# Kernel optimization log

Hardware: AMD Instinct MI355X
Metric: run time of the kernel (lower is better)

## Reference

```python
import jax, jax.numpy as jnp
import numpy as np

B = 4096
FEAT = 40960
HID = 1024
L1 = 64
L2 = 32
P_ACTIVE = 30.0 / FEAT  # ~30 active features per position


def setup_inputs() -> dict:
    key = jax.random.key(0)
    ks = jax.random.split(key, 12)
    # Sparse binary HalfKP-style features
    white_features = (jax.random.uniform(ks[0], (B, FEAT)) < P_ACTIVE).astype(jnp.float32)
    black_features = (jax.random.uniform(ks[1], (B, FEAT)) < P_ACTIVE).astype(jnp.float32)
    stm = (jax.random.uniform(ks[2], (B, 1)) < 0.5).astype(jnp.float32)
    s = 0.02
    params = {
        'ft_w': jax.random.normal(ks[3], (HID, FEAT), jnp.float32) * s,
        'ft_b': jax.random.normal(ks[4], (HID,), jnp.float32) * s,
        'l1_w': jax.random.normal(ks[5], (L1, 2 * HID), jnp.float32) * s,
        'l1_b': jax.random.normal(ks[6], (L1,), jnp.float32) * s,
        'l2_w': jax.random.normal(ks[7], (L2, L1), jnp.float32) * s,
        'l2_b': jax.random.normal(ks[8], (L2,), jnp.float32) * s,
        'l3_w': jax.random.normal(ks[9], (1, L2), jnp.float32) * s,
        'l3_b': jax.random.normal(ks[10], (1,), jnp.float32) * s,
    }
    return dict(white_features=white_features, black_features=black_features, stm=stm, **params)


def reference(white_features, black_features, stm,
              ft_w, ft_b, l1_w, l1_b, l2_w, l2_b, l3_w, l3_b):
    # Feature transformer (shared weights, both perspectives)
    w = white_features @ ft_w.T + ft_b  # [B, HID]
    b = black_features @ ft_w.T + ft_b  # [B, HID]
    wb = jnp.concatenate([w, b], axis=1)  # [B, 2*HID]
    bw = jnp.concatenate([b, w], axis=1)
    acc = stm * wb + (1.0 - stm) * bw
    h1 = jnp.clip(acc, 0.0, 1.0)
    h2 = jnp.clip(h1 @ l1_w.T + l1_b, 0.0, 1.0)
    h3 = jnp.clip(h2 @ l2_w.T + l2_b, 0.0, 1.0)
    raw = h3 @ l3_w.T + l3_b  # [B, 1]
    return jax.nn.sigmoid(raw), raw
```

## Files before the change

kernel.cpp:

```cpp
#include <hip/hip_runtime.h>
#include <hip/hip_bf16.h>

#define B_SZ 4096
#define FEAT 40960
#define HID  1024
#define L1N  64
#define L2N  32
#define IDX_CAP 512

static __device__ __forceinline__ unsigned short f2bf(float x) {
    __hip_bfloat16 h = __float2bfloat16(x);
    return *reinterpret_cast<unsigned short*>(&h);
}
static __device__ __forceinline__ float bf2f(unsigned short u) {
    unsigned int v = ((unsigned int)u) << 16;
    return __uint_as_float(v);
}
static __device__ __forceinline__ float clipf(float x) {
    return fminf(fmaxf(x, 0.0f), 1.0f);
}

__global__ __launch_bounds__(256) void transpose_ftw(
    const float* __restrict__ ftw, unsigned short* __restrict__ ftwT) {
    __shared__ float tile[32][33];
    int tx = threadIdx.x, ty = threadIdx.y;
    int f0 = blockIdx.x * 32;
    int h0 = blockIdx.y * 32;
#pragma unroll
    for (int i = 0; i < 4; ++i) {
        int h = h0 + ty + 8 * i;
        tile[ty + 8 * i][tx] = ftw[(size_t)h * FEAT + f0 + tx];
    }
    __syncthreads();
#pragma unroll
    for (int i = 0; i < 4; ++i) {
        int f = f0 + ty + 8 * i;
        ftwT[(size_t)f * HID + h0 + tx] = f2bf(tile[tx][ty + 8 * i]);
    }
}

__global__ __launch_bounds__(256) void ft_kernel(
    const float* __restrict__ wf, const float* __restrict__ bfeat,
    const float* __restrict__ stm, const unsigned short* __restrict__ ftwT,
    const float* __restrict__ ftb, unsigned short* __restrict__ h1) {

    __shared__ int w_idx[IDX_CAP];
    __shared__ int b_idx[IDX_CAP];
    __shared__ int cnt_w, cnt_b;

    const int t = threadIdx.x;
    const int b = blockIdx.x;

    if (t == 0) { cnt_w = 0; cnt_b = 0; }
    __syncthreads();

    const float4* wf4 = (const float4*)(wf + (size_t)b * FEAT);
    const float4* bf4 = (const float4*)(bfeat + (size_t)b * FEAT);
    for (int it = 0; it < (FEAT / 4) / 256; ++it) {
        int i4 = it * 256 + t;
        float4 wv = wf4[i4];
        float4 bv = bf4[i4];
        int base = i4 * 4;
        if (wv.x != 0.f) { int p = atomicAdd(&cnt_w, 1); if (p < IDX_CAP) w_idx[p] = base + 0; }
        if (wv.y != 0.f) { int p = atomicAdd(&cnt_w, 1); if (p < IDX_CAP) w_idx[p] = base + 1; }
        if (wv.z != 0.f) { int p = atomicAdd(&cnt_w, 1); if (p < IDX_CAP) w_idx[p] = base + 2; }
        if (wv.w != 0.f) { int p = atomicAdd(&cnt_w, 1); if (p < IDX_CAP) w_idx[p] = base + 3; }
        if (bv.x != 0.f) { int p = atomicAdd(&cnt_b, 1); if (p < IDX_CAP) b_idx[p] = base + 0; }
        if (bv.y != 0.f) { int p = atomicAdd(&cnt_b, 1); if (p < IDX_CAP) b_idx[p] = base + 1; }
        if (bv.z != 0.f) { int p = atomicAdd(&cnt_b, 1); if (p < IDX_CAP) b_idx[p] = base + 2; }
        if (bv.w != 0.f) { int p = atomicAdd(&cnt_b, 1); if (p < IDX_CAP) b_idx[p] = base + 3; }
    }
    __syncthreads();
    const int nw = min(cnt_w, IDX_CAP);
    const int nb = min(cnt_b, IDX_CAP);

    float4 bias = ((const float4*)ftb)[t];
    float aw0 = bias.x, aw1 = bias.y, aw2 = bias.z, aw3 = bias.w;
    float ab0 = bias.x, ab1 = bias.y, ab2 = bias.z, ab3 = bias.w;

    for (int i = 0; i < nw; ++i) {
        int f = w_idx[i];
        ushort4 u = ((const ushort4*)(ftwT + (size_t)f * HID))[t];
        aw0 += bf2f(u.x); aw1 += bf2f(u.y); aw2 += bf2f(u.z); aw3 += bf2f(u.w);
    }
    for (int i = 0; i < nb; ++i) {
        int f = b_idx[i];
        ushort4 u = ((const ushort4*)(ftwT + (size_t)f * HID))[t];
        ab0 += bf2f(u.x); ab1 += bf2f(u.y); ab2 += bf2f(u.z); ab3 += bf2f(u.w);
    }

    const bool wfirst = (stm[b] != 0.0f);
    float f0 = wfirst ? aw0 : ab0, f1 = wfirst ? aw1 : ab1;
    float f2 = wfirst ? aw2 : ab2, f3 = wfirst ? aw3 : ab3;
    float s0 = wfirst ? ab0 : aw0, s1 = wfirst ? ab1 : aw1;
    float s2 = wfirst ? ab2 : aw2, s3 = wfirst ? ab3 : aw3;

    ushort4 of, os;
    of.x = f2bf(clipf(f0)); of.y = f2bf(clipf(f1)); of.z = f2bf(clipf(f2)); of.w = f2bf(clipf(f3));
    os.x = f2bf(clipf(s0)); os.y = f2bf(clipf(s1)); os.z = f2bf(clipf(s2)); os.w = f2bf(clipf(s3));

    ((ushort4*)(h1 + (size_t)b * 2 * HID))[t]       = of;
    ((ushort4*)(h1 + (size_t)b * 2 * HID + HID))[t] = os;
}

__global__ __launch_bounds__(256) void mlp_kernel(
    const unsigned short* __restrict__ h1,
    const float* __restrict__ l1w, const float* __restrict__ l1b,
    const float* __restrict__ l2w, const float* __restrict__ l2b,
    const float* __restrict__ l3w, const float* __restrict__ l3b,
    float* __restrict__ out) {

    const int ROWS = 4;
    __shared__ float  h1s[4][2 * HID];
    __shared__ float4 part[4 * L1N];
    __shared__ float  h2s[4][L1N];
    __shared__ float  h3s[4][L2N];

    const int t = threadIdx.x;
    const int r0 = blockIdx.x * ROWS;

    for (int r = 0; r < ROWS; ++r) {
        const ushort4* src = (const ushort4*)(h1 + (size_t)(r0 + r) * 2 * HID);
        ushort4 u0 = src[t];
        ushort4 u1 = src[256 + t];
        h1s[r][4 * t + 0] = bf2f(u0.x); h1s[r][4 * t + 1] = bf2f(u0.y);
        h1s[r][4 * t + 2] = bf2f(u0.z); h1s[r][4 * t + 3] = bf2f(u0.w);
        h1s[r][1024 + 4 * t + 0] = bf2f(u1.x); h1s[r][1024 + 4 * t + 1] = bf2f(u1.y);
        h1s[r][1024 + 4 * t + 2] = bf2f(u1.z); h1s[r][1024 + 4 * t + 3] = bf2f(u1.w);
    }
    __syncthreads();

    {
        const int k = t & 63, p = t >> 6;
        float a0 = 0.f, a1 = 0.f, a2 = 0.f, a3 = 0.f;
        const float4* w4 = (const float4*)(l1w + (size_t)k * 2 * HID + (size_t)p * 512);
        const int jbase = p * 512;
        for (int jj = 0; jj < 128; ++jj) {
            float4 w = w4[jj];
            int j = jbase + jj * 4;
            a0 += w.x * h1s[0][j] + w.y * h1s[0][j + 1] + w.z * h1s[0][j + 2] + w.w * h1s[0][j + 3];
            a1 += w.x * h1s[1][j] + w.y * h1s[1][j + 1] + w.z * h1s[1][j + 2] + w.w * h1s[1][j + 3];
            a2 += w.x * h1s[2][j] + w.y * h1s[2][j + 1] + w.z * h1s[2][j + 2] + w.w * h1s[2][j + 3];
            a3 += w.x * h1s[3][j] + w.y * h1s[3][j + 1] + w.z * h1s[3][j + 2] + w.w * h1s[3][j + 3];
        }
        part[p * L1N + k] = make_float4(a0, a1, a2, a3);
    }
    __syncthreads();
    if (t < L1N) {
        float4 s0 = part[t], s1 = part[L1N + t], s2 = part[2 * L1N + t], s3 = part[3 * L1N + t];
        float bias = l1b[t];
        h2s[0][t] = clipf(s0.x + s1.x + s2.x + s3.x + bias);
        h2s[1][t] = clipf(s0.y + s1.y + s2.y + s3.y + bias);
        h2s[2][t] = clipf(s0.z + s1.z + s2.z + s3.z + bias);
        h2s[3][t] = clipf(s0.w + s1.w + s2.w + s3.w + bias);
    }
    __syncthreads();

    if (t < ROWS * L2N) {
        int r = t >> 5, k2 = t & 31;
        float a = l2b[k2];
        for (int j = 0; j < L1N; ++j) a += h2s[r][j] * l2w[k2 * L1N + j];
        h3s[r][k2] = clipf(a);
    }
    __syncthreads();

    if (t < ROWS) {
        float raw = l3b[0];
        for (int j = 0; j < L2N; ++j) raw += h3s[t][j] * l3w[j];
        float sig = 1.0f / (1.0f + expf(-raw));
        out[r0 + t] = sig;
        out[B_SZ + r0 + t] = raw;
    }
}

extern "C" void kernel_launch(void* const* d_in, const int* in_sizes, int n_in,
                              void* d_out, int out_size, void* d_ws, size_t ws_size,
                              hipStream_t stream) {
    const float* wf    = (const float*)d_in[0];
    const float* bfeat = (const float*)d_in[1];
    const float* stm   = (const float*)d_in[2];
    const float* ftw   = (const float*)d_in[3];
    const float* ftb   = (const float*)d_in[4];
    const float* l1w   = (const float*)d_in[5];
    const float* l1b   = (const float*)d_in[6];
    const float* l2w   = (const float*)d_in[7];
    const float* l2b   = (const float*)d_in[8];
    const float* l3w   = (const float*)d_in[9];
    const float* l3b   = (const float*)d_in[10];
    float* out = (float*)d_out;

    unsigned short* ftwT = (unsigned short*)d_ws;
    unsigned short* h1   = ftwT + (size_t)FEAT * HID;

    transpose_ftw<<<dim3(FEAT / 32, HID / 32), dim3(32, 8), 0, stream>>>(ftw, ftwT);
    ft_kernel<<<B_SZ, 256, 0, stream>>>(wf, bfeat, stm, ftwT, ftb, h1);
    mlp_kernel<<<B_SZ / 4, 256, 0, stream>>>(h1, l1w, l1b, l2w, l2b, l3w, l3b, out);
}
```

Baseline: 1.459 ms.

## Fuse feature transformer with MLP and widen transpose tiles with packed bf16 stores

The sparse feature-transformer kernel and the MLP kernel are merged into one kernel that handles four rows per block, so the bf16 h1 intermediate is kept in shared memory in fp32 instead of being written to and re-read from global memory. The transpose kernel now uses 32x64 tiles and writes packed pairs of bf16 values as 32-bit stores. The fused kernel has a quarter as many blocks as the old feature-transformer kernel, and each block scans four rows serially. This lowers parallelism and raises shared-memory use, which could hurt latency hiding on the memory-bound feature scan. IDX_CAP is also reduced to 128 indices per row.

After: 1.515 ms. 1.04x slower.

```diff
diff --git a/kernel.cpp b/kernel.cpp
--- a/kernel.cpp
+++ b/kernel.cpp
@@ -6,7 +6,8 @@
 #define HID  1024
 #define L1N  64
 #define L2N  32
-#define IDX_CAP 512
+#define IDX_CAP 128
+#define ROWS 4
 
 static __device__ __forceinline__ unsigned short f2bf(float x) {
     __hip_bfloat16 h = __float2bfloat16(x);
@@ -22,111 +23,101 @@
 
 __global__ __launch_bounds__(256) void transpose_ftw(
     const float* __restrict__ ftw, unsigned short* __restrict__ ftwT) {
-    __shared__ float tile[32][33];
-    int tx = threadIdx.x, ty = threadIdx.y;
-    int f0 = blockIdx.x * 32;
-    int h0 = blockIdx.y * 32;
+    __shared__ float tile[32][65];
+    const int tx = threadIdx.x;
+    const int ty = threadIdx.y;
+    const int f0 = blockIdx.x * 32;
+    const int h0 = blockIdx.y * 64;
 #pragma unroll
-    for (int i = 0; i < 4; ++i) {
-        int h = h0 + ty + 8 * i;
-        tile[ty + 8 * i][tx] = ftw[(size_t)h * FEAT + f0 + tx];
+    for (int i = 0; i < 8; ++i) {
+        int h = ty + 8 * i;
+        tile[tx][h] = ftw[(size_t)(h0 + h) * FEAT + f0 + tx];
     }
     __syncthreads();
 #pragma unroll
     for (int i = 0; i < 4; ++i) {
-        int f = f0 + ty + 8 * i;
-        ftwT[(size_t)f * HID + h0 + tx] = f2bf(tile[tx][ty + 8 * i]);
+        int f = ty + 8 * i;
+        float a = tile[f][2 * tx];
+        float b = tile[f][2 * tx + 1];
+        unsigned int pk = (unsigned int)f2bf(a) | ((unsigned int)f2bf(b) << 16);
+        ((unsigned int*)(ftwT + (size_t)(f0 + f) * HID + h0))[tx] = pk;
     }
 }
 
-__global__ __launch_bounds__(256) void ft_kernel(
+__global__ __launch_bounds__(256) void nnue_fused(
     const float* __restrict__ wf, const float* __restrict__ bfeat,
     const float* __restrict__ stm, const unsigned short* __restrict__ ftwT,
-    const float* __restrict__ ftb, unsigned short* __restrict__ h1) {
-
-    __shared__ int w_idx[IDX_CAP];
-    __shared__ int b_idx[IDX_CAP];
-    __shared__ int cnt_w, cnt_b;
-
-    const int t = threadIdx.x;
-    const int b = blockIdx.x;
-
-    if (t == 0) { cnt_w = 0; cnt_b = 0; }
-    __syncthreads();
-
-    const float4* wf4 = (const float4*)(wf + (size_t)b * FEAT);
-    const float4* bf4 = (const float4*)(bfeat + (size_t)b * FEAT);
-    for (int it = 0; it < (FEAT / 4) / 256; ++it) {
-        int i4 = it * 256 + t;
-        float4 wv = wf4[i4];
-        float4 bv = bf4[i4];
-        int base = i4 * 4;
-        if (wv.x != 0.f) { int p = atomicAdd(&cnt_w, 1); if (p < IDX_CAP) w_idx[p] = base + 0; }
-        if (wv.y != 0.f) { int p = atomicAdd(&cnt_w, 1); if (p < IDX_CAP) w_idx[p] = base + 1; }
-        if (wv.z != 0.f) { int p = atomicAdd(&cnt_w, 1); if (p < IDX_CAP) w_idx[p] = base + 2; }
-        if (wv.w != 0.f) { int p = atomicAdd(&cnt_w, 1); if (p < IDX_CAP) w_idx[p] = base + 3; }
-        if (bv.x != 0.f) { int p = atomicAdd(&cnt_b, 1); if (p < IDX_CAP) b_idx[p] = base + 0; }
-        if (bv.y != 0.f) { int p = atomicAdd(&cnt_b, 1); if (p < IDX_CAP) b_idx[p] = base + 1; }
-        if (bv.z != 0.f) { int p = atomicAdd(&cnt_b, 1); if (p < IDX_CAP) b_idx[p] = base + 2; }
-        if (bv.w != 0.f) { int p = atomicAdd(&cnt_b, 1); if (p < IDX_CAP) b_idx[p] = base + 3; }
-    }
-    __syncthreads();
-    const int nw = min(cnt_w, IDX_CAP);
-    const int nb = min(cnt_b, IDX_CAP);
-
-    float4 bias = ((const float4*)ftb)[t];
-    float aw0 = bias.x, aw1 = bias.y, aw2 = bias.z, aw3 = bias.w;
-    float ab0 = bias.x, ab1 = bias.y, ab2 = bias.z, ab3 = bias.w;
-
-    for (int i = 0; i < nw; ++i) {
-        int f = w_idx[i];
-        ushort4 u = ((const ushort4*)(ftwT + (size_t)f * HID))[t];
-        aw0 += bf2f(u.x); aw1 += bf2f(u.y); aw2 += bf2f(u.z); aw3 += bf2f(u.w);
-    }
-    for (int i = 0; i < nb; ++i) {
-        int f = b_idx[i];
-        ushort4 u = ((const ushort4*)(ftwT + (size_t)f * HID))[t];
-        ab0 += bf2f(u.x); ab1 += bf2f(u.y); ab2 += bf2f(u.z); ab3 += bf2f(u.w);
-    }
-
-    const bool wfirst = (stm[b] != 0.0f);
-    float f0 = wfirst ? aw0 : ab0, f1 = wfirst ? aw1 : ab1;
-    float f2 = wfirst ? aw2 : ab2, f3 = wfirst ? aw3 : ab3;
-    float s0 = wfirst ? ab0 : aw0, s1 = wfirst ? ab1 : aw1;
-    float s2 = wfirst ? ab2 : aw2, s3 = wfirst ? ab3 : aw3;
-
-    ushort4 of, os;
-    of.x = f2bf(clipf(f0)); of.y = f2bf(clipf(f1)); of.z = f2bf(clipf(f2)); of.w = f2bf(clipf(f3));
-    os.x = f2bf(clipf(s0)); os.y = f2bf(clipf(s1)); os.z = f2bf(clipf(s2)); os.w = f2bf(clipf(s3));
-
-    ((ushort4*)(h1 + (size_t)b * 2 * HID))[t]       = of;
-    ((ushort4*)(h1 + (size_t)b * 2 * HID + HID))[t] = os;
-}
-
-__global__ __launch_bounds__(256) void mlp_kernel(
-    const unsigned short* __restrict__ h1,
+    const float* __restrict__ ftb,
     const float* __restrict__ l1w, const float* __restrict__ l1b,
     const float* __restrict__ l2w, const float* __restrict__ l2b,
     const float* __restrict__ l3w, const float* __restrict__ l3b,
     float* __restrict__ out) {
 
-    const int ROWS = 4;
-    __shared__ float  h1s[4][2 * HID];
+    __shared__ int  idx[2][ROWS][IDX_CAP];
+    __shared__ int  cnt[2][ROWS];
+    __shared__ float h1s[ROWS][2 * HID];
     __shared__ float4 part[4 * L1N];
-    __shared__ float  h2s[4][L1N];
-    __shared__ float  h3s[4][L2N];
+    __shared__ float h2s[ROWS][L1N];
+    __shared__ float h3s[ROWS][L2N];
 
     const int t = threadIdx.x;
     const int r0 = blockIdx.x * ROWS;
 
+    if (t < 2 * ROWS) ((int*)cnt)[t] = 0;
+    __syncthreads();
+
     for (int r = 0; r < ROWS; ++r) {
-        const ushort4* src = (const ushort4*)(h1 + (size_t)(r0 + r) * 2 * HID);
-        ushort4 u0 = src[t];
-        ushort4 u1 = src[256 + t];
-        h1s[r][4 * t + 0] = bf2f(u0.x); h1s[r][4 * t + 1] = bf2f(u0.y);
-        h1s[r][4 * t + 2] = bf2f(u0.z); h1s[r][4 * t + 3] = bf2f(u0.w);
-        h1s[r][1024 + 4 * t + 0] = bf2f(u1.x); h1s[r][1024 + 4 * t + 1] = bf2f(u1.y);
-        h1s[r][1024 + 4 * t + 2] = bf2f(u1.z); h1s[r][1024 + 4 * t + 3] = bf2f(u1.w);
+        const float4* wf4 = (const float4*)(wf + (size_t)(r0 + r) * FEAT);
+        const float4* bf4 = (const float4*)(bfeat + (size_t)(r0 + r) * FEAT);
+        for (int it = 0; it < (FEAT / 4) / 256; ++it) {
+            int i4 = it * 256 + t;
+            float4 wv = wf4[i4];
+            float4 bv = bf4[i4];
+            int base = i4 * 4;
+            if (wv.x != 0.f) { int p = atomicAdd(&cnt[0][r], 1); if (p < IDX_CAP) idx[0][r][p] = base + 0; }
+            if (wv.y != 0.f) { int p = atomicAdd(&cnt[0][r], 1); if (p < IDX_CAP) idx[0][r][p] = base + 1; }
+            if (wv.z != 0.f) { int p = atomicAdd(&cnt[0][r], 1); if (p < IDX_CAP) idx[0][r][p] = base + 2; }
+            if (wv.w != 0.f) { int p = atomicAdd(&cnt[0][r], 1); if (p < IDX_CAP) idx[0][r][p] = base + 3; }
+            if (bv.x != 0.f) { int p = atomicAdd(&cnt[1][r], 1); if (p < IDX_CAP) idx[1][r][p] = base + 0; }
+            if (bv.y != 0.f) { int p = atomicAdd(&cnt[1][r], 1); if (p < IDX_CAP) idx[1][r][p] = base + 1; }
+            if (bv.z != 0.f) { int p = atomicAdd(&cnt[1][r], 1); if (p < IDX_CAP) idx[1][r][p] = base + 2; }
+            if (bv.w != 0.f) { int p = atomicAdd(&cnt[1][r], 1); if (p < IDX_CAP) idx[1][r][p] = base + 3; }
+        }
+    }
+    __syncthreads();
+
+    float4 bias = ((const float4*)ftb)[t];
+    float aw[ROWS][4], ab[ROWS][4];
+#pragma unroll
+    for (int r = 0; r < ROWS; ++r) {
+        aw[r][0] = bias.x; aw[r][1] = bias.y; aw[r][2] = bias.z; aw[r][3] = bias.w;
+        ab[r][0] = bias.x; ab[r][1] = bias.y; ab[r][2] = bias.z; ab[r][3] = bias.w;
+    }
+#pragma unroll
+    for (int pp = 0; pp < 2; ++pp) {
+        for (int r = 0; r < ROWS; ++r) {
+            const int n = min(cnt[pp][r], IDX_CAP);
+            float* acc = pp ? ab[r] : aw[r];
+#pragma unroll 4
+            for (int i = 0; i < n; ++i) {
+                int f = idx[pp][r][i];
+                ushort4 u = ((const ushort4*)(ftwT + (size_t)f * HID))[t];
+                acc[0] += bf2f(u.x); acc[1] += bf2f(u.y);
+                acc[2] += bf2f(u.z); acc[3] += bf2f(u.w);
+            }
+        }
+    }
+
+#pragma unroll
+    for (int r = 0; r < ROWS; ++r) {
+        const bool wfirst = (stm[r0 + r] != 0.0f);
+#pragma unroll
+        for (int c = 0; c < 4; ++c) {
+            float fst = wfirst ? aw[r][c] : ab[r][c];
+            float snd = wfirst ? ab[r][c] : aw[r][c];
+            h1s[r][4 * t + c]       = clipf(fst);
+            h1s[r][HID + 4 * t + c] = clipf(snd);
+        }
     }
     __syncthreads();
 
@@ -148,11 +139,11 @@
     __syncthreads();
     if (t < L1N) {
         float4 s0 = part[t], s1 = part[L1N + t], s2 = part[2 * L1N + t], s3 = part[3 * L1N + t];
-        float bias = l1b[t];
-        h2s[0][t] = clipf(s0.x + s1.x + s2.x + s3.x + bias);
-        h2s[1][t] = clipf(s0.y + s1.y + s2.y + s3.y + bias);
-        h2s[2][t] = clipf(s0.z + s1.z + s2.z + s3.z + bias);
-        h2s[3][t] = clipf(s0.w + s1.w + s2.w + s3.w + bias);
+        float b1 = l1b[t];
+        h2s[0][t] = clipf(s0.x + s1.x + s2.x + s3.x + b1);
+        h2s[1][t] = clipf(s0.y + s1.y + s2.y + s3.y + b1);
+        h2s[2][t] = clipf(s0.z + s1.z + s2.z + s3.z + b1);
+        h2s[3][t] = clipf(s0.w + s1.w + s2.w + s3.w + b1);
     }
     __syncthreads();
 
@@ -167,8 +158,7 @@
     if (t < ROWS) {
         float raw = l3b[0];
         for (int j = 0; j < L2N; ++j) raw += h3s[t][j] * l3w[j];
-        float sig = 1.0f / (1.0f + expf(-raw));
-        out[r0 + t] = sig;
+        out[r0 + t] = 1.0f / (1.0f + expf(-raw));
         out[B_SZ + r0 + t] = raw;
     }
 }
@@ -190,9 +180,8 @@
     float* out = (float*)d_out;
 
     unsigned short* ftwT = (unsigned short*)d_ws;
-    unsigned short* h1   = ftwT + (size_t)FEAT * HID;
 
-    transpose_ftw<<<dim3(FEAT / 32, HID / 32), dim3(32, 8), 0, stream>>>(ftw, ftwT);
-    ft_kernel<<<B_SZ, 256, 0, stream>>>(wf, bfeat, stm, ftwT, ftb, h1);
-    mlp_kernel<<<B_SZ / 4, 256, 0, stream>>>(h1, l1w, l1b, l2w, l2b, l3w, l3b, out);
+    transpose_ftw<<<dim3(FEAT / 32, HID / 64), dim3(32, 8), 0, stream>>>(ftw, ftwT);
+    nnue_fused<<<B_SZ / ROWS, 256, 0, stream>>>(wf, bfeat, stm, ftwT, ftb,
+                                                l1w, l1b, l2w, l2b, l3w, l3b, out);
 }
```
